# Kernel optimization log

Measured on AMD Instinct MI355X. Metric: run time of the kernel, lower is better.

The kernel has to match this reference:

```python
import jax, jax.numpy as jnp
import numpy as np

N, E, G, F_IN, H, C = 50000, 800000, 512, 128, 96, 10
BN_EPS = 1e-5


def _bn(x, w, b):
    # torch BatchNorm1d training-mode forward: batch stats, biased variance
    mu = jnp.mean(x, axis=0)
    var = jnp.var(x, axis=0)
    return (x - mu) * jax.lax.rsqrt(var + BN_EPS) * w + b


def setup_inputs() -> dict:
    key = jax.random.key(0)
    ks = iter(jax.random.split(key, 64))

    def rn(shape, s=0.05):
        return jax.random.normal(next(ks), shape, jnp.float32) * s

    inp = {
        "x": jax.random.normal(next(ks), (N, F_IN), jnp.float32),
        "edge_index": jax.random.randint(next(ks), (2, E), 0, N, dtype=jnp.int32),
        "batch": jnp.sort(jax.random.randint(next(ks), (N,), 0, G, dtype=jnp.int32)),
        "bn_feat_w": jnp.ones((F_IN,), jnp.float32),
        "bn_feat_b": jnp.full((F_IN,), 1e-4, jnp.float32),
        "Wf": rn((F_IN, H)), "bf": jnp.zeros((H,), jnp.float32),
        "bn_fc_w": jnp.ones((H,), jnp.float32),
        "bn_fc_b": jnp.full((H,), 1e-4, jnp.float32),
        "Wl": rn((H, H)), "bl": jnp.zeros((H,), jnp.float32),
        "bn_hid_w": jnp.ones((H,), jnp.float32),
        "bn_hid_b": jnp.full((H,), 1e-4, jnp.float32),
        "Wc": rn((H, C)), "bc": jnp.zeros((C,), jnp.float32),
    }
    for i in range(3):
        inp[f"W1_{i}"] = rn((H, H)); inp[f"b1_{i}"] = jnp.zeros((H,), jnp.float32)
        inp[f"bnw_{i}"] = jnp.ones((H,), jnp.float32)
        inp[f"bnb_{i}"] = jnp.full((H,), 1e-4, jnp.float32)
        inp[f"W2_{i}"] = rn((H, H)); inp[f"b2_{i}"] = jnp.zeros((H,), jnp.float32)
    return inp


def reference(x, edge_index, batch, bn_feat_w, bn_feat_b, Wf, bf,
              W1_0, b1_0, bnw_0, bnb_0, W2_0, b2_0,
              W1_1, b1_1, bnw_1, bnb_1, W2_1, b2_1,
              W1_2, b1_2, bnw_2, bnb_2, W2_2, b2_2,
              bn_fc_w, bn_fc_b, Wl, bl, bn_hid_w, bn_hid_b, Wc, bc):
    src, dst = edge_index[0], edge_index[1]
    h = _bn(x, bn_feat_w, bn_feat_b)
    # GCNConv(gfn=True): pure linear feature transform, no propagation
    h = jax.nn.relu(h @ Wf + bf)
    gin_params = [
        (W1_0, b1_0, bnw_0, bnb_0, W2_0, b2_0),
        (W1_1, b1_1, bnw_1, bnb_1, W2_1, b2_1),
        (W1_2, b1_2, bnw_2, bnb_2, W2_2, b2_2),
    ]
    for W1, b1, bw, bb, W2, b2 in gin_params:
        # GIN: (1+eps)*x + sum-aggregate of neighbor features (eps=0)
        agg = jax.ops.segment_sum(h[src], dst, num_segments=N)  # [N, H]
        m = h + agg
        m = jax.nn.relu(_bn(m @ W1 + b1, bw, bb))
        h = jax.nn.relu(m @ W2 + b2)
    # global_add_pool over graphs
    g = jax.ops.segment_sum(h, batch, num_segments=G)  # [G, H]
    g = jax.nn.relu(_bn(g, bn_fc_w, bn_fc_b) @ Wl + bl)
    g = _bn(g, bn_hid_w, bn_hid_b)
    logits = g @ Wc + bc
    return jax.nn.log_softmax(logits, axis=-1)
```

## Files before the change

### kernel.cpp

```cpp
#include <hip/hip_runtime.h>

#define N_NODES 50000
#define N_EDGES 800000
#define N_GRAPHS 512
#define F_IN 128
#define HDIM 96
#define NCLS 10
#define BN_EPS 1e-5f

#define NPB 128
#define NBUCK2 ((N_NODES + NPB - 1) / NPB)
#define NEB 128
#define EPB ((N_EDGES + NEB - 1) / NEB)

typedef unsigned int u32;
typedef unsigned short u16;
typedef __attribute__((ext_vector_type(8))) short bf16x8;
typedef __attribute__((ext_vector_type(4))) float f32x4;

__device__ __forceinline__ u16 f2bf(float f) {
    u32 u = __float_as_uint(f);
    u32 r = (u + 0x7fffu + ((u >> 16) & 1u)) >> 16;
    return (u16)r;
}
__device__ __forceinline__ float bflo(u32 w) { return __uint_as_float(w << 16); }
__device__ __forceinline__ float bfhi(u32 w) { return __uint_as_float(w & 0xffff0000u); }

template<int NC>
__global__ __launch_bounds__(256) void colstats4_kernel(const float* __restrict__ in,
                                                        float* __restrict__ stats,
                                                        int nrows) {
    constexpr int CG  = NC / 4;
    constexpr int RPB = 256 / CG;
    const int cg = threadIdx.x % CG;
    const int rg = threadIdx.x / CG;
    float4 s = make_float4(0.f, 0.f, 0.f, 0.f);
    float4 q = make_float4(0.f, 0.f, 0.f, 0.f);
    for (int r = blockIdx.x * RPB + rg; r < nrows; r += gridDim.x * RPB) {
        float4 v = *(const float4*)&in[(size_t)r * NC + cg * 4];
        s.x += v.x; s.y += v.y; s.z += v.z; s.w += v.w;
        q.x += v.x * v.x; q.y += v.y * v.y; q.z += v.z * v.z; q.w += v.w * v.w;
    }
    __shared__ float ss[RPB][NC], sq[RPB][NC];
    *(float4*)&ss[rg][cg * 4] = s;
    *(float4*)&sq[rg][cg * 4] = q;
    __syncthreads();
    if (threadIdx.x < NC) {
        float a = 0.f, b = 0.f;
        #pragma unroll
        for (int r = 0; r < RPB; r++) { a += ss[r][threadIdx.x]; b += sq[r][threadIdx.x]; }
        atomicAdd(&stats[threadIdx.x],      a);
        atomicAdd(&stats[NC + threadIdx.x], b);
    }
}

template<int NC>
__global__ __launch_bounds__(2*NC) void colstats_kernel(const float* __restrict__ in,
                                                        float* __restrict__ stats,
                                                        int nrows) {
    const int col  = threadIdx.x % NC;
    const int half = threadIdx.x / NC;
    float s = 0.f, ss = 0.f;
    for (int r = blockIdx.x * 2 + half; r < nrows; r += gridDim.x * 2) {
        float v = in[(size_t)r * NC + col];
        s += v; ss += v * v;
    }
    __shared__ float shs[2][NC], shq[2][NC];
    shs[half][col] = s; shq[half][col] = ss;
    __syncthreads();
    if (half == 0) {
        atomicAdd(&stats[col],      s  + shs[1][col]);
        atomicAdd(&stats[NC + col], ss + shq[1][col]);
    }
}

__global__ void finalize_bn_kernel(const float* __restrict__ stats,
                                   const float* __restrict__ w,
                                   const float* __restrict__ b,
                                   float* __restrict__ ac, int ncols, float inv_n) {
    int k = blockIdx.x * blockDim.x + threadIdx.x;
    if (k < ncols) {
        float mu  = stats[k] * inv_n;
        float var = stats[ncols + k] * inv_n - mu * mu;
        float a   = w[k] * rsqrtf(var + BN_EPS);
        ac[k]         = a;
        ac[ncols + k] = b[k] - mu * a;
    }
}

template<int KDIM, bool FOLD>
__global__ __launch_bounds__(256) void wprep_kernel(const float* __restrict__ W,
                                                    const float* __restrict__ bias,
                                                    const float* __restrict__ ac,
                                                    u16* __restrict__ wtb,
                                                    float* __restrict__ bmod) {
    int i = blockIdx.x * 256 + threadIdx.x;
    if (i < KDIM * 96) {
        int k = i / 96, n = i % 96;
        float v = W[i];
        if constexpr (FOLD) v *= ac[k];
        wtb[n * KDIM + k] = f2bf(v);
    }
    if (blockIdx.x == 0 && threadIdx.x < 96) {
        float b = bias[threadIdx.x];
        if constexpr (FOLD) {
            for (int k = 0; k < KDIM; k++) b += ac[KDIM + k] * W[k * 96 + threadIdx.x];
        }
        bmod[threadIdx.x] = b;
    }
}

__global__ __launch_bounds__(1024) void scan1_kernel(const int* __restrict__ in,
                                                     int* __restrict__ tmp,
                                                     int* __restrict__ partial, int n) {
    __shared__ int sh[1024];
    const int i = blockIdx.x * 1024 + threadIdx.x;
    const int d = (i < n) ? in[i] : 0;
    sh[threadIdx.x] = d;
    __syncthreads();
    for (int off = 1; off < 1024; off <<= 1) {
        int v = 0;
        if (threadIdx.x >= off) v = sh[threadIdx.x - off];
        __syncthreads();
        sh[threadIdx.x] += v;
        __syncthreads();
    }
    if (i < n) tmp[i] = sh[threadIdx.x] - d;
    if (threadIdx.x == 1023) partial[blockIdx.x] = sh[1023];
}

__global__ void scan2_kernel(int* __restrict__ partial, int nparts) {
    const int t = threadIdx.x;
    int d = (t < nparts) ? partial[t] : 0;
    int v = d;
    for (int off = 1; off < 64; off <<= 1) {
        int u = __shfl_up(v, off, 64);
        if (t >= off) v += u;
    }
    if (t < nparts) partial[t] = v - d;
}

__global__ __launch_bounds__(1024) void scan3_rowptr_kernel(const int* __restrict__ tmp,
                                                            const int* __restrict__ partial,
                                                            const int* __restrict__ deg,
                                                            int* __restrict__ row_ptr, int n) {
    const int i = blockIdx.x * 1024 + threadIdx.x;
    if (i < n) {
        int v = tmp[i] + partial[blockIdx.x];
        row_ptr[i] = v;
        if (i == n - 1) row_ptr[n] = v + deg[i];
    }
}

__global__ __launch_bounds__(1024) void scan3_kernel(const int* __restrict__ tmp,
                                                     const int* __restrict__ partial,
                                                     int* __restrict__ out, int n) {
    const int i = blockIdx.x * 1024 + threadIdx.x;
    if (i < n) out[i] = tmp[i] + partial[blockIdx.x];
}

__global__ __launch_bounds__(256) void count_kernel(const int* __restrict__ dst,
                                                    int* __restrict__ deg,
                                                    int* __restrict__ cnt ) {
    __shared__ int lc[NBUCK2];
    for (int i = threadIdx.x; i < NBUCK2; i += 256) lc[i] = 0;
    __syncthreads();
    const int lo = blockIdx.x * EPB;
    const int hi = min(lo + EPB, N_EDGES);
    for (int e = lo + threadIdx.x; e < hi; e += 256) {
        int d = dst[e];
        atomicAdd(&lc[d / NPB], 1);
        atomicAdd(&deg[d], 1);
    }
    __syncthreads();
    for (int i = threadIdx.x; i < NBUCK2; i += 256)
        cnt[i * NEB + blockIdx.x] = lc[i];
}

__global__ __launch_bounds__(256) void distribute_kernel(const int* __restrict__ src,
                                                         const int* __restrict__ dst,
                                                         const int* __restrict__ ofs,
                                                         u32* __restrict__ ebuf) {
    __shared__ int lofs[NBUCK2];
    for (int i = threadIdx.x; i < NBUCK2; i += 256) lofs[i] = ofs[i * NEB + blockIdx.x];
    __syncthreads();
    const int lo = blockIdx.x * EPB;
    const int hi = min(lo + EPB, N_EDGES);
    for (int e = lo + threadIdx.x; e < hi; e += 256) {
        int d = dst[e];
        int q = atomicAdd(&lofs[d / NPB], 1);
        ebuf[q] = ((u32)src[e] << 7) | (u32)(d & (NPB - 1));
    }
}

__global__ __launch_bounds__(256) void bucket_fill_kernel(const u32* __restrict__ ebuf,
                                                          const int* __restrict__ ofs,
                                                          const int* __restrict__ row_ptr,
                                                          int* __restrict__ csr) {
    __shared__ int cur[NPB];
    const int p    = blockIdx.x;
    const int base = p * NPB;
    const int nn   = min(NPB, N_NODES - base);
    for (int i = threadIdx.x; i < nn; i += 256) cur[i] = row_ptr[base + i];
    __syncthreads();
    const int e0 = ofs[p * NEB];
    const int e1 = (p + 1 < NBUCK2) ? ofs[(p + 1) * NEB] : N_EDGES;
    for (int e = e0 + threadIdx.x; e < e1; e += 256) {
        u32 v = ebuf[e];
        int pos = atomicAdd(&cur[v & (NPB - 1)], 1);
        csr[pos] = (int)(v >> 7);
    }
}

__global__ __launch_bounds__(192) void agg_kernel(const u16* __restrict__ hb,
                                                  const int* __restrict__ row_ptr,
                                                  const int* __restrict__ csr,
                                                  u16* __restrict__ mb, int n) {
    const int jj   = threadIdx.x % 12;
    const int node = blockIdx.x * 16 + threadIdx.x / 12;
    if (node >= n) return;
    const int p0 = row_ptr[node], p1 = row_ptr[node + 1];
    uint4 sv = *(const uint4*)&hb[(size_t)node * 96 + jj * 8];
    float a0 = bflo(sv.x), a1 = bfhi(sv.x), a2 = bflo(sv.y), a3 = bfhi(sv.y);
    float a4 = bflo(sv.z), a5 = bfhi(sv.z), a6 = bflo(sv.w), a7 = bfhi(sv.w);
    int p = p0;
    for (; p + 8 <= p1; p += 8) {
        int s0 = csr[p],     s1 = csr[p + 1], s2 = csr[p + 2], s3 = csr[p + 3];
        int s4 = csr[p + 4], s5 = csr[p + 5], s6 = csr[p + 6], s7 = csr[p + 7];
        uint4 v0 = *(const uint4*)&hb[(size_t)s0 * 96 + jj * 8];
        uint4 v1 = *(const uint4*)&hb[(size_t)s1 * 96 + jj * 8];
        uint4 v2 = *(const uint4*)&hb[(size_t)s2 * 96 + jj * 8];
        uint4 v3 = *(const uint4*)&hb[(size_t)s3 * 96 + jj * 8];
        uint4 v4 = *(const uint4*)&hb[(size_t)s4 * 96 + jj * 8];
        uint4 v5 = *(const uint4*)&hb[(size_t)s5 * 96 + jj * 8];
        uint4 v6 = *(const uint4*)&hb[(size_t)s6 * 96 + jj * 8];
        uint4 v7 = *(const uint4*)&hb[(size_t)s7 * 96 + jj * 8];
        a0 += ((bflo(v0.x) + bflo(v1.x)) + (bflo(v2.x) + bflo(v3.x)))
            + ((bflo(v4.x) + bflo(v5.x)) + (bflo(v6.x) + bflo(v7.x)));
        a1 += ((bfhi(v0.x) + bfhi(v1.x)) + (bfhi(v2.x) + bfhi(v3.x)))
            + ((bfhi(v4.x) + bfhi(v5.x)) + (bfhi(v6.x) + bfhi(v7.x)));
        a2 += ((bflo(v0.y) + bflo(v1.y)) + (bflo(v2.y) + bflo(v3.y)))
            + ((bflo(v4.y) + bflo(v5.y)) + (bflo(v6.y) + bflo(v7.y)));
        a3 += ((bfhi(v0.y) + bfhi(v1.y)) + (bfhi(v2.y) + bfhi(v3.y)))
            + ((bfhi(v4.y) + bfhi(v5.y)) + (bfhi(v6.y) + bfhi(v7.y)));
        a4 += ((bflo(v0.z) + bflo(v1.z)) + (bflo(v2.z) + bflo(v3.z)))
            + ((bflo(v4.z) + bflo(v5.z)) + (bflo(v6.z) + bflo(v7.z)));
        a5 += ((bfhi(v0.z) + bfhi(v1.z)) + (bfhi(v2.z) + bfhi(v3.z)))
            + ((bfhi(v4.z) + bfhi(v5.z)) + (bfhi(v6.z) + bfhi(v7.z)));
        a6 += ((bflo(v0.w) + bflo(v1.w)) + (bflo(v2.w) + bflo(v3.w)))
            + ((bflo(v4.w) + bflo(v5.w)) + (bflo(v6.w) + bflo(v7.w)));
        a7 += ((bfhi(v0.w) + bfhi(v1.w)) + (bfhi(v2.w) + bfhi(v3.w)))
            + ((bfhi(v4.w) + bfhi(v5.w)) + (bfhi(v6.w) + bfhi(v7.w)));
    }
    for (; p + 4 <= p1; p += 4) {
        int s0 = csr[p], s1 = csr[p + 1], s2 = csr[p + 2], s3 = csr[p + 3];
        uint4 v0 = *(const uint4*)&hb[(size_t)s0 * 96 + jj * 8];
        uint4 v1 = *(const uint4*)&hb[(size_t)s1 * 96 + jj * 8];
        uint4 v2 = *(const uint4*)&hb[(size_t)s2 * 96 + jj * 8];
        uint4 v3 = *(const uint4*)&hb[(size_t)s3 * 96 + jj * 8];
        a0 += (bflo(v0.x) + bflo(v1.x)) + (bflo(v2.x) + bflo(v3.x));
        a1 += (bfhi(v0.x) + bfhi(v1.x)) + (bfhi(v2.x) + bfhi(v3.x));
        a2 += (bflo(v0.y) + bflo(v1.y)) + (bflo(v2.y) + bflo(v3.y));
        a3 += (bfhi(v0.y) + bfhi(v1.y)) + (bfhi(v2.y) + bfhi(v3.y));
        a4 += (bflo(v0.z) + bflo(v1.z)) + (bflo(v2.z) + bflo(v3.z));
        a5 += (bfhi(v0.z) + bfhi(v1.z)) + (bfhi(v2.z) + bfhi(v3.z));
        a6 += (bflo(v0.w) + bflo(v1.w)) + (bflo(v2.w) + bflo(v3.w));
        a7 += (bfhi(v0.w) + bfhi(v1.w)) + (bfhi(v2.w) + bfhi(v3.w));
    }
    for (; p < p1; p++) {
        int s = csr[p];
        uint4 v = *(const uint4*)&hb[(size_t)s * 96 + jj * 8];
        a0 += bflo(v.x); a1 += bfhi(v.x); a2 += bflo(v.y); a3 += bfhi(v.y);
        a4 += bflo(v.z); a5 += bfhi(v.z); a6 += bflo(v.w); a7 += bfhi(v.w);
    }
    uint4 o;
    o.x = (u32)f2bf(a0) | ((u32)f2bf(a1) << 16);
    o.y = (u32)f2bf(a2) | ((u32)f2bf(a3) << 16);
    o.z = (u32)f2bf(a4) | ((u32)f2bf(a5) << 16);
    o.w = (u32)f2bf(a6) | ((u32)f2bf(a7) << 16);
    *(uint4*)&mb[(size_t)node * 96 + jj * 8] = o;
}

template<int KDIM, bool IN_F32, bool IN_AFF_RELU, bool OUT_RELU, bool STATS, bool OUT_BF16, bool POOL>
__global__ __launch_bounds__(256) void mmx_kernel(const void* __restrict__ in_,
                                                  const u16* __restrict__ wt,
                                                  const float* __restrict__ bias,
                                                  const float* __restrict__ ac,
                                                  void* __restrict__ out_,
                                                  float* __restrict__ stats,
                                                  const int* __restrict__ batch,
                                                  int nrows) {
    constexpr int KP = KDIM + 8;
    constexpr int KB = KDIM / 32;
    __shared__ u16 wlds[96 * KP];
    __shared__ u16 alds[64 * KP];
    __shared__ float sred[2][4][96];
    const int tid = threadIdx.x;

    for (int i = tid; i < 96 * (KDIM / 8); i += 256) {
        int nn = i / (KDIM / 8), c8 = i % (KDIM / 8);
        *(uint4*)&wlds[nn * KP + c8 * 8] = *(const uint4*)&wt[nn * KDIM + c8 * 8];
    }

    const int w    = tid >> 6;
    const int lane = tid & 63;
    const int r16  = lane & 15;
    const int kg   = lane >> 4;
    const int m0   = w * 16;
    float bn[6];
    #pragma unroll
    for (int nt = 0; nt < 6; nt++) bn[nt] = bias[nt * 16 + r16];
    float scol[6] = {0,0,0,0,0,0}, qcol[6] = {0,0,0,0,0,0};

    const int nchunks = (nrows + 63) / 64;
    for (int chunk = blockIdx.x; chunk < nchunks; chunk += gridDim.x) {
        const int row0 = chunk * 64;
        __syncthreads();
        if constexpr (IN_F32) {
            const float* inf = (const float*)in_;
            for (int i = tid; i < 64 * (KDIM / 4); i += 256) {
                int r = i / (KDIM / 4), c4 = i % (KDIM / 4);
                int gr = row0 + r;
                float4 v = (gr < nrows) ? *(const float4*)&inf[(size_t)gr * KDIM + c4 * 4]
                                        : make_float4(0.f, 0.f, 0.f, 0.f);
                ushort4 o; o.x = f2bf(v.x); o.y = f2bf(v.y); o.z = f2bf(v.z); o.w = f2bf(v.w);
                *(ushort4*)&alds[r * KP + c4 * 4] = o;
            }
        } else {
            const u16* inb = (const u16*)in_;
            for (int i = tid; i < 64 * (KDIM / 8); i += 256) {
                int r = i / (KDIM / 8), c8 = i % (KDIM / 8);
                int gr = row0 + r;
                uint4 v = (gr < nrows) ? *(const uint4*)&inb[(size_t)gr * KDIM + c8 * 8]
                                       : make_uint4(0u, 0u, 0u, 0u);
                if constexpr (IN_AFF_RELU) {
                    u32 words[4] = {v.x, v.y, v.z, v.w};
                    #pragma unroll
                    for (int t2 = 0; t2 < 4; t2++) {
                        int k0 = c8 * 8 + t2 * 2;
                        float lo = fmaxf(bflo(words[t2]) * ac[k0]     + ac[KDIM + k0],     0.f);
                        float hi = fmaxf(bfhi(words[t2]) * ac[k0 + 1] + ac[KDIM + k0 + 1], 0.f);
                        words[t2] = (u32)f2bf(lo) | ((u32)f2bf(hi) << 16);
                    }
                    v.x = words[0]; v.y = words[1]; v.z = words[2]; v.w = words[3];
                }
                *(uint4*)&alds[r * KP + c8 * 8] = v;
            }
        }
        __syncthreads();

        bf16x8 af[KB];
        #pragma unroll
        for (int kb = 0; kb < KB; kb++)
            af[kb] = *(const bf16x8*)&alds[(m0 + r16) * KP + kb * 32 + kg * 8];

        f32x4 acc[6];
        #pragma unroll
        for (int nt = 0; nt < 6; nt++) acc[nt] = (f32x4){bn[nt], bn[nt], bn[nt], bn[nt]};
        #pragma unroll
        for (int kb = 0; kb < KB; kb++) {
            #pragma unroll
            for (int nt = 0; nt < 6; nt++) {
                bf16x8 bfr = *(const bf16x8*)&wlds[(nt * 16 + r16) * KP + kb * 32 + kg * 8];
                acc[nt] = __builtin_amdgcn_mfma_f32_16x16x32_bf16(af[kb], bfr, acc[nt], 0, 0, 0);
            }
        }

        const int gr0  = row0 + m0 + kg * 4;
        const bool full = (gr0 + 3 < nrows);
        if constexpr (POOL) {
            float* gbuf = (float*)out_;
            int bl = -1, bh = -2;
            if (full) { bl = batch[gr0]; bh = batch[gr0 + 3]; }
            #pragma unroll
            for (int nt = 0; nt < 6; nt++) {
                float v0 = acc[nt][0], v1 = acc[nt][1], v2 = acc[nt][2], v3 = acc[nt][3];
                if constexpr (OUT_RELU) {
                    v0 = fmaxf(v0, 0.f); v1 = fmaxf(v1, 0.f);
                    v2 = fmaxf(v2, 0.f); v3 = fmaxf(v3, 0.f);
                }
                const int n = nt * 16 + r16;
                if (full) {
                    if (bl == bh) {
                        atomicAdd(&gbuf[(size_t)bl * 96 + n], (v0 + v1) + (v2 + v3));
                    } else {
                        atomicAdd(&gbuf[(size_t)batch[gr0]     * 96 + n], v0);
                        atomicAdd(&gbuf[(size_t)batch[gr0 + 1] * 96 + n], v1);
                        atomicAdd(&gbuf[(size_t)batch[gr0 + 2] * 96 + n], v2);
                        atomicAdd(&gbuf[(size_t)batch[gr0 + 3] * 96 + n], v3);
                    }
                } else {
                    if (gr0     < nrows) atomicAdd(&gbuf[(size_t)batch[gr0]     * 96 + n], v0);
                    if (gr0 + 1 < nrows) atomicAdd(&gbuf[(size_t)batch[gr0 + 1] * 96 + n], v1);
                    if (gr0 + 2 < nrows) atomicAdd(&gbuf[(size_t)batch[gr0 + 2] * 96 + n], v2);
                }
            }
        } else {
            #pragma unroll
            for (int nt = 0; nt < 6; nt++) {
                float v[4] = {acc[nt][0], acc[nt][1], acc[nt][2], acc[nt][3]};
                if constexpr (OUT_RELU) {
                    #pragma unroll
                    for (int rr = 0; rr < 4; rr++) v[rr] = fmaxf(v[rr], 0.f);
                }
                const int n = nt * 16 + r16;
                #pragma unroll
                for (int rr = 0; rr < 4; rr++) {
                    const int gr = gr0 + rr;
                    if (full || gr < nrows) {
                        if constexpr (OUT_BF16) ((u16*)out_)[(size_t)gr * 96 + n] = f2bf(v[rr]);
                        else                    ((float*)out_)[(size_t)gr * 96 + n] = v[rr];
                        if constexpr (STATS) { scol[nt] += v[rr]; qcol[nt] += v[rr] * v[rr]; }
                    }
                }
            }
        }
    }

    if constexpr (STATS) {
        #pragma unroll
        for (int nt = 0; nt < 6; nt++) {
            scol[nt] += __shfl_xor(scol[nt], 16);
            scol[nt] += __shfl_xor(scol[nt], 32);
            qcol[nt] += __shfl_xor(qcol[nt], 16);
            qcol[nt] += __shfl_xor(qcol[nt], 32);
        }
        __syncthreads();
        if (kg == 0) {
            #pragma unroll
            for (int nt = 0; nt < 6; nt++) {
                sred[0][w][nt * 16 + r16] = scol[nt];
                sred[1][w][nt * 16 + r16] = qcol[nt];
            }
        }
        __syncthreads();
        if (tid < 96) {
            float a = sred[0][0][tid] + sred[0][1][tid] + sred[0][2][tid] + sred[0][3][tid];
            float b = sred[1][0][tid] + sred[1][1][tid] + sred[1][2][tid] + sred[1][3][tid];
            atomicAdd(&stats[tid],      a);
            atomicAdd(&stats[96 + tid], b);
        }
    }
}

template<int KDIM, bool IN_AFF, bool IN_RELU, bool OUT_RELU, bool STATS>
__global__ __launch_bounds__(192) void mm_kernel(const float* __restrict__ in,
                                                 const float* __restrict__ W,
                                                 const float* __restrict__ bias,
                                                 const float* __restrict__ ac,
                                                 float* __restrict__ out,
                                                 float* __restrict__ stats, int nrows) {
    constexpr int KG = KDIM / 4;
    __shared__ float ws[KDIM][96];
    __shared__ float xs[32][KDIM];
    const int tid = threadIdx.x;
    const int cg  = tid % 24;
    const int rg  = tid / 24;
    for (int i = tid; i < KDIM * 24; i += 192) {
        int k = i / 24, c4 = i % 24;
        *(float4*)&ws[k][c4 * 4] = *(const float4*)&W[(size_t)k * 96 + c4 * 4];
    }
    const float4 bj = *(const float4*)&bias[cg * 4];
    float s0=0,s1=0,s2=0,s3=0, q0=0,q1=0,q2=0,q3=0;
    const int nchunks = (nrows + 31) / 32;
    for (int chunk = blockIdx.x; chunk < nchunks; chunk += gridDim.x) {
        const int row0 = chunk * 32;
        __syncthreads();
        for (int i = tid; i < 32 * KG; i += 192) {
            int r = i / KG, g = i % KG;
            int gr = row0 + r;
            float4 v = make_float4(0.f, 0.f, 0.f, 0.f);
            if (gr < nrows) v = *(const float4*)&in[(size_t)gr * KDIM + g * 4];
            if constexpr (IN_AFF) {
                float4 a = *(const float4*)&ac[g * 4];
                float4 c = *(const float4*)&ac[KDIM + g * 4];
                v.x = v.x * a.x + c.x; v.y = v.y * a.y + c.y;
                v.z = v.z * a.z + c.z; v.w = v.w * a.w + c.w;
            }
            if constexpr (IN_RELU) {
                v.x = fmaxf(v.x, 0.f); v.y = fmaxf(v.y, 0.f);
                v.z = fmaxf(v.z, 0.f); v.w = fmaxf(v.w, 0.f);
            }
            *(float4*)&xs[r][4 * (g ^ (r & 7))] = v;
        }
        __syncthreads();
        float acc[4][4];
        #pragma unroll
        for (int m = 0; m < 4; m++) {
            acc[m][0] = bj.x; acc[m][1] = bj.y; acc[m][2] = bj.z; acc[m][3] = bj.w;
        }
        #pragma unroll 4
        for (int g = 0; g < KG; g++) {
            const int xi = 4 * (g ^ rg);
            float4 xv0 = *(const float4*)&xs[rg     ][xi];
            float4 xv1 = *(const float4*)&xs[rg +  8][xi];
            float4 xv2 = *(const float4*)&xs[rg + 16][xi];
            float4 xv3 = *(const float4*)&xs[rg + 24][xi];
            #pragma unroll
            for (int i = 0; i < 4; i++) {
                float4 wv = *(const float4*)&ws[g * 4 + i][cg * 4];
                float x0 = (i==0)?xv0.x:(i==1)?xv0.y:(i==2)?xv0.z:xv0.w;
                float x1 = (i==0)?xv1.x:(i==1)?xv1.y:(i==2)?xv1.z:xv1.w;
                float x2 = (i==0)?xv2.x:(i==1)?xv2.y:(i==2)?xv2.z:xv2.w;
                float x3 = (i==0)?xv3.x:(i==1)?xv3.y:(i==2)?xv3.z:xv3.w;
                acc[0][0] = fmaf(x0, wv.x, acc[0][0]); acc[0][1] = fmaf(x0, wv.y, acc[0][1]);
                acc[0][2] = fmaf(x0, wv.z, acc[0][2]); acc[0][3] = fmaf(x0, wv.w, acc[0][3]);
                acc[1][0] = fmaf(x1, wv.x, acc[1][0]); acc[1][1] = fmaf(x1, wv.y, acc[1][1]);
                acc[1][2] = fmaf(x1, wv.z, acc[1][2]); acc[1][3] = fmaf(x1, wv.w, acc[1][3]);
                acc[2][0] = fmaf(x2, wv.x, acc[2][0]); acc[2][1] = fmaf(x2, wv.y, acc[2][1]);
                acc[2][2] = fmaf(x2, wv.z, acc[2][2]); acc[2][3] = fmaf(x2, wv.w, acc[2][3]);
                acc[3][0] = fmaf(x3, wv.x, acc[3][0]); acc[3][1] = fmaf(x3, wv.y, acc[3][1]);
                acc[3][2] = fmaf(x3, wv.z, acc[3][2]); acc[3][3] = fmaf(x3, wv.w, acc[3][3]);
            }
        }
        #pragma unroll
        for (int m = 0; m < 4; m++) {
            const int gr = row0 + rg + 8 * m;
            if (gr < nrows) {
                float4 o = make_float4(acc[m][0], acc[m][1], acc[m][2], acc[m][3]);
                if constexpr (OUT_RELU) {
                    o.x = fmaxf(o.x, 0.f); o.y = fmaxf(o.y, 0.f);
                    o.z = fmaxf(o.z, 0.f); o.w = fmaxf(o.w, 0.f);
                }
                *(float4*)&out[(size_t)gr * 96 + cg * 4] = o;
                if constexpr (STATS) {
                    s0 += o.x; q0 += o.x * o.x; s1 += o.y; q1 += o.y * o.y;
                    s2 += o.z; q2 += o.z * o.z; s3 += o.w; q3 += o.w * o.w;
                }
            }
        }
    }
    if constexpr (STATS) {
        __syncthreads();
        float* rs = &xs[0][0];
        float* rq = rs + 8 * 96;
        rs[rg * 96 + cg * 4 + 0] = s0; rs[rg * 96 + cg * 4 + 1] = s1;
        rs[rg * 96 + cg * 4 + 2] = s2; rs[rg * 96 + cg * 4 + 3] = s3;
        rq[rg * 96 + cg * 4 + 0] = q0; rq[rg * 96 + cg * 4 + 1] = q1;
        rq[rg * 96 + cg * 4 + 2] = q2; rq[rg * 96 + cg * 4 + 3] = q3;
        __syncthreads();
        if (tid < 96) {
            float a = 0.f, b = 0.f;
            #pragma unroll
            for (int r = 0; r < 8; r++) { a += rs[r * 96 + tid]; b += rq[r * 96 + tid]; }
            atomicAdd(&stats[tid],      a);
            atomicAdd(&stats[96 + tid], b);
        }
    }
}

__global__ void head_kernel(const float* __restrict__ g1, const float* __restrict__ ac,
                            const float* __restrict__ Wc, const float* __restrict__ bc,
                            float* __restrict__ out, int ngraphs) {
    int gi = blockIdx.x * blockDim.x + threadIdx.x;
    if (gi >= ngraphs) return;
    float v[NCLS];
    #pragma unroll
    for (int c = 0; c < NCLS; c++) v[c] = bc[c];
    for (int k = 0; k < HDIM; k++) {
        float x = g1[(size_t)gi * HDIM + k] * ac[k] + ac[HDIM + k];
        #pragma unroll
        for (int c = 0; c < NCLS; c++) v[c] = fmaf(x, Wc[k * NCLS + c], v[c]);
    }
    float mx = v[0];
    #pragma unroll
    for (int c = 1; c < NCLS; c++) mx = fmaxf(mx, v[c]);
    float sum = 0.f;
    #pragma unroll
    for (int c = 0; c < NCLS; c++) sum += expf(v[c] - mx);
    float lse = mx + logf(sum);
    #pragma unroll
    for (int c = 0; c < NCLS; c++) out[(size_t)gi * NCLS + c] = v[c] - lse;
}

extern "C" void kernel_launch(void* const* d_in, const int* in_sizes, int n_in,
                              void* d_out, int out_size, void* d_ws, size_t ws_size,
                              hipStream_t stream) {
    const float* x         = (const float*)d_in[0];
    const int*   ei        = (const int*)  d_in[1];
    const int*   batch     = (const int*)  d_in[2];
    const float* bn_feat_w = (const float*)d_in[3];
    const float* bn_feat_b = (const float*)d_in[4];
    const float* Wf        = (const float*)d_in[5];
    const float* bfv       = (const float*)d_in[6];
    const float* bn_fc_w   = (const float*)d_in[7];
    const float* bn_fc_b   = (const float*)d_in[8];
    const float* Wl        = (const float*)d_in[9];
    const float* bl        = (const float*)d_in[10];
    const float* bn_hid_w  = (const float*)d_in[11];
    const float* bn_hid_b  = (const float*)d_in[12];
    const float* Wc        = (const float*)d_in[13];
    const float* bc        = (const float*)d_in[14];
    float* out = (float*)d_out;

    char* p = (char*)d_ws;
    auto alloc = [&](size_t bytes) { char* q = p; p += (bytes + 255) & ~(size_t)255; return q; };
    u16*   hb     = (u16*)  alloc((size_t)N_NODES * HDIM * 2);
    u16*   mb     = (u16*)  alloc((size_t)N_NODES * HDIM * 2);
    float* g      = (float*)alloc((size_t)N_GRAPHS * HDIM * 4);
    float* g1     = (float*)alloc((size_t)N_GRAPHS * HDIM * 4);
    float* statsX = (float*)alloc(2 * F_IN * 4);
    float* acX    = (float*)alloc(2 * F_IN * 4);
    float* statsT = (float*)alloc(2 * HDIM * 4);
    float* acT    = (float*)alloc(2 * HDIM * 4);
    float* statsG = (float*)alloc(2 * HDIM * 4);
    float* acG    = (float*)alloc(2 * HDIM * 4);
    float* statsG1= (float*)alloc(2 * HDIM * 4);
    float* acHid  = (float*)alloc(2 * HDIM * 4);
    u16*   wtF    = (u16*)  alloc(96 * F_IN * 2);
    float* bFmod  = (float*)alloc(96 * 4);
    u16*   wt1[3]; u16* wt2[3]; float* b1mod[3]; float* b2mod[3];
    for (int l = 0; l < 3; l++) {
        wt1[l] = (u16*)alloc(96 * HDIM * 2); b1mod[l] = (float*)alloc(96 * 4);
        wt2[l] = (u16*)alloc(96 * HDIM * 2); b2mod[l] = (float*)alloc(96 * 4);
    }
    int* deg      = (int*)alloc((size_t)N_NODES * 4);
    int* row_ptr  = (int*)alloc((size_t)(N_NODES + 1) * 4);
    int* csr      = (int*)alloc((size_t)N_EDGES * 4);
    int* stmp     = (int*)alloc((size_t)N_NODES * 4);
    int* spart    = (int*)alloc(64 * 4);
    int* cnt      = (int*)alloc((size_t)NBUCK2 * NEB * 4);
    int* ofs      = (int*)alloc((size_t)NBUCK2 * NEB * 4);
    int* stmp2    = (int*)alloc((size_t)NBUCK2 * NEB * 4);
    int* spart2   = (int*)alloc(64 * 4);
    u32* ebuf     = (u32*)alloc((size_t)N_EDGES * 4);

    const int* srcp = ei;
    const int* dstp = ei + N_EDGES;

    const int nch64  = (N_NODES + 63) / 64;
    const int gridF  = (nch64 < 768) ? nch64 : 768;
    const int grid96 = (nch64 < 1024) ? nch64 : 1024;
    const int gridG  = (N_GRAPHS + 31) / 32;
    const int nscan  = (N_NODES + 1023) / 1024;
    const int ncb    = NBUCK2 * NEB;
    const int nscan2 = (ncb + 1023) / 1024;

    hipMemsetAsync(statsX, 0, 2 * F_IN * 4, stream);
    colstats4_kernel<F_IN><<<256, 256, 0, stream>>>(x, statsX, N_NODES);
    finalize_bn_kernel<<<1, F_IN, 0, stream>>>(statsX, bn_feat_w, bn_feat_b, acX, F_IN, 1.0f / N_NODES);
    wprep_kernel<F_IN, true><<<(F_IN * 96 + 255) / 256, 256, 0, stream>>>(Wf, bfv, acX, wtF, bFmod);
    mmx_kernel<F_IN, true, false, true, false, true, false><<<gridF, 256, 0, stream>>>(x, wtF, bFmod, nullptr, hb, nullptr, nullptr, N_NODES);

    for (int l = 0; l < 3; l++) {
        wprep_kernel<HDIM, false><<<(HDIM * 96 + 255) / 256, 256, 0, stream>>>((const float*)d_in[15 + 6 * l], (const float*)d_in[16 + 6 * l], nullptr, wt1[l], b1mod[l]);
        wprep_kernel<HDIM, false><<<(HDIM * 96 + 255) / 256, 256, 0, stream>>>((const float*)d_in[19 + 6 * l], (const float*)d_in[20 + 6 * l], nullptr, wt2[l], b2mod[l]);
    }

    hipMemsetAsync(deg, 0, (size_t)N_NODES * 4, stream);
    count_kernel<<<NEB, 256, 0, stream>>>(dstp, deg, cnt);
    scan1_kernel<<<nscan, 1024, 0, stream>>>(deg, stmp, spart, N_NODES);
    scan2_kernel<<<1, 64, 0, stream>>>(spart, nscan);
    scan3_rowptr_kernel<<<nscan, 1024, 0, stream>>>(stmp, spart, deg, row_ptr, N_NODES);
    scan1_kernel<<<nscan2, 1024, 0, stream>>>(cnt, stmp2, spart2, ncb);
    scan2_kernel<<<1, 64, 0, stream>>>(spart2, nscan2);
    scan3_kernel<<<nscan2, 1024, 0, stream>>>(stmp2, spart2, ofs, ncb);
    distribute_kernel<<<NEB, 256, 0, stream>>>(srcp, dstp, ofs, ebuf);
    bucket_fill_kernel<<<NBUCK2, 256, 0, stream>>>(ebuf, ofs, row_ptr, csr);

    hipMemsetAsync(g, 0, (size_t)N_GRAPHS * HDIM * 4, stream);

    for (int l = 0; l < 3; l++) {
        const float* bw = (const float*)d_in[17 + 6 * l];
        const float* bb = (const float*)d_in[18 + 6 * l];
        agg_kernel<<<(N_NODES + 15) / 16, 192, 0, stream>>>(hb, row_ptr, csr, mb, N_NODES);
        hipMemsetAsync(statsT, 0, 2 * HDIM * 4, stream);
        mmx_kernel<HDIM, false, false, false, true, true, false><<<grid96, 256, 0, stream>>>(mb, wt1[l], b1mod[l], nullptr, mb, statsT, nullptr, N_NODES);
        finalize_bn_kernel<<<1, HDIM, 0, stream>>>(statsT, bw, bb, acT, HDIM, 1.0f / N_NODES);
        if (l < 2) {
            mmx_kernel<HDIM, false, true, true, false, true, false><<<grid96, 256, 0, stream>>>(mb, wt2[l], b2mod[l], acT, hb, nullptr, nullptr, N_NODES);
        } else {
            mmx_kernel<HDIM, false, true, true, false, false, true><<<grid96, 256, 0, stream>>>(mb, wt2[l], b2mod[l], acT, g, nullptr, batch, N_NODES);
        }
    }

    hipMemsetAsync(statsG, 0, 2 * HDIM * 4, stream);
    colstats_kernel<HDIM><<<64, 2 * HDIM, 0, stream>>>(g, statsG, N_GRAPHS);
    finalize_bn_kernel<<<1, HDIM, 0, stream>>>(statsG, bn_fc_w, bn_fc_b, acG, HDIM, 1.0f / N_GRAPHS);
    hipMemsetAsync(statsG1, 0, 2 * HDIM * 4, stream);
    mm_kernel<HDIM, true, false, true, true><<<gridG, 192, 0, stream>>>(g, Wl, bl, acG, g1, statsG1, N_GRAPHS);
    finalize_bn_kernel<<<1, HDIM, 0, stream>>>(statsG1, bn_hid_w, bn_hid_b, acHid, HDIM, 1.0f / N_GRAPHS);

    head_kernel<<<2, 256, 0, stream>>>(g1, acHid, Wc, bc, out, N_GRAPHS);
}
```

Measured before the change: 371.5 us.

## Merge weight-prep launches, fold scan2 into scan3, coalesce memsets, fp32 intermediate

All seven weight-prep launches become one kernel. The separate scan2 kernels go away: each scan3 block sums the preceding partials with a wavefront reduction. All zeroing memsets are grouped into one contiguous region cleared once, with per-layer stats buffers. The first GIN matmul now writes fp32 into a new buffer instead of bf16 in place, and the second matmul reads fp32 and applies the BN affine plus ReLU during load. Fewer launches cut host overhead, but the intermediate activation traffic doubles from bf16 to fp32.

```diff
diff --git a/kernel.cpp b/kernel.cpp
--- a/kernel.cpp
+++ b/kernel.cpp
@@ -88,26 +88,53 @@
     }
 }
 
-template<int KDIM, bool FOLD>
-__global__ __launch_bounds__(256) void wprep_kernel(const float* __restrict__ W,
-                                                    const float* __restrict__ bias,
-                                                    const float* __restrict__ ac,
-                                                    u16* __restrict__ wtb,
-                                                    float* __restrict__ bmod) {
-    int i = blockIdx.x * 256 + threadIdx.x;
-    if (i < KDIM * 96) {
+#define WPF_BLOCKS 48
+#define WPH_BLOCKS 36
+__global__ __launch_bounds__(256) void wprep_all_kernel(
+        const float* __restrict__ Wf, const float* __restrict__ bf, const float* __restrict__ acX,
+        const float* __restrict__ W0a, const float* __restrict__ b0a,
+        const float* __restrict__ W0b, const float* __restrict__ b0b,
+        const float* __restrict__ W1a, const float* __restrict__ b1a,
+        const float* __restrict__ W1b, const float* __restrict__ b1b,
+        const float* __restrict__ W2a, const float* __restrict__ b2a,
+        const float* __restrict__ W2b, const float* __restrict__ b2b,
+        u16* __restrict__ wtF, float* __restrict__ bFm,
+        u16* __restrict__ wtbase, float* __restrict__ bmbase) {
+    const int tid = threadIdx.x;
+    int blk = blockIdx.x;
+    if (blk < WPF_BLOCKS) {
+        int i = blk * 256 + tid;
+        if (i < F_IN * 96) {
+            int k = i / 96, n = i % 96;
+            wtF[n * F_IN + k] = f2bf(Wf[i] * acX[k]);
+        }
+        if (blk == 0 && tid < 96) {
+            float b = bf[tid];
+            for (int k = 0; k < F_IN; k++) b += acX[F_IN + k] * Wf[k * 96 + tid];
+            bFm[tid] = b;
+        }
+        return;
+    }
+    blk -= WPF_BLOCKS;
+    const int s  = blk / WPH_BLOCKS;
+    const int b2 = blk % WPH_BLOCKS;
+    const float* W; const float* bias;
+    switch (s) {
+        case 0: W = W0a; bias = b0a; break;
+        case 1: W = W0b; bias = b0b; break;
+        case 2: W = W1a; bias = b1a; break;
+        case 3: W = W1b; bias = b1b; break;
+        case 4: W = W2a; bias = b2a; break;
+        default: W = W2b; bias = b2b; break;
+    }
+    u16*   wtb  = wtbase + (size_t)s * 96 * HDIM;
+    float* bmod = bmbase + (size_t)s * 96;
+    int i = b2 * 256 + tid;
+    if (i < HDIM * 96) {
         int k = i / 96, n = i % 96;
-        float v = W[i];
-        if constexpr (FOLD) v *= ac[k];
-        wtb[n * KDIM + k] = f2bf(v);
-    }
-    if (blockIdx.x == 0 && threadIdx.x < 96) {
-        float b = bias[threadIdx.x];
-        if constexpr (FOLD) {
-            for (int k = 0; k < KDIM; k++) b += ac[KDIM + k] * W[k * 96 + threadIdx.x];
-        }
-        bmod[threadIdx.x] = b;
-    }
+        wtb[n * HDIM + k] = f2bf(W[i]);
+    }
+    if (b2 == 0 && tid < 96) bmod[tid] = bias[tid];
 }
 
 __global__ __launch_bounds__(1024) void scan1_kernel(const int* __restrict__ in,
@@ -129,24 +156,21 @@
     if (threadIdx.x == 1023) partial[blockIdx.x] = sh[1023];
 }
 
-__global__ void scan2_kernel(int* __restrict__ partial, int nparts) {
-    const int t = threadIdx.x;
-    int d = (t < nparts) ? partial[t] : 0;
-    int v = d;
-    for (int off = 1; off < 64; off <<= 1) {
-        int u = __shfl_up(v, off, 64);
-        if (t >= off) v += u;
-    }
-    if (t < nparts) partial[t] = v - d;
-}
-
 __global__ __launch_bounds__(1024) void scan3_rowptr_kernel(const int* __restrict__ tmp,
                                                             const int* __restrict__ partial,
                                                             const int* __restrict__ deg,
-                                                            int* __restrict__ row_ptr, int n) {
+                                                            int* __restrict__ row_ptr,
+                                                            int n, int nparts) {
+    __shared__ int offs;
+    if (threadIdx.x < 64) {
+        int v = (threadIdx.x < blockIdx.x && threadIdx.x < nparts) ? partial[threadIdx.x] : 0;
+        for (int o = 32; o > 0; o >>= 1) v += __shfl_down(v, o, 64);
+        if (threadIdx.x == 0) offs = v;
+    }
+    __syncthreads();
     const int i = blockIdx.x * 1024 + threadIdx.x;
     if (i < n) {
-        int v = tmp[i] + partial[blockIdx.x];
+        int v = tmp[i] + offs;
         row_ptr[i] = v;
         if (i == n - 1) row_ptr[n] = v + deg[i];
     }
@@ -154,14 +178,22 @@
 
 __global__ __launch_bounds__(1024) void scan3_kernel(const int* __restrict__ tmp,
                                                      const int* __restrict__ partial,
-                                                     int* __restrict__ out, int n) {
+                                                     int* __restrict__ out,
+                                                     int n, int nparts) {
+    __shared__ int offs;
+    if (threadIdx.x < 64) {
+        int v = (threadIdx.x < blockIdx.x && threadIdx.x < nparts) ? partial[threadIdx.x] : 0;
+        for (int o = 32; o > 0; o >>= 1) v += __shfl_down(v, o, 64);
+        if (threadIdx.x == 0) offs = v;
+    }
+    __syncthreads();
     const int i = blockIdx.x * 1024 + threadIdx.x;
-    if (i < n) out[i] = tmp[i] + partial[blockIdx.x];
+    if (i < n) out[i] = tmp[i] + offs;
 }
 
 __global__ __launch_bounds__(256) void count_kernel(const int* __restrict__ dst,
                                                     int* __restrict__ deg,
-                                                    int* __restrict__ cnt ) {
+                                                    int* __restrict__ cnt) {
     __shared__ int lc[NBUCK2];
     for (int i = threadIdx.x; i < NBUCK2; i += 256) lc[i] = 0;
     __syncthreads();
@@ -323,6 +355,14 @@
                 int gr = row0 + r;
                 float4 v = (gr < nrows) ? *(const float4*)&inf[(size_t)gr * KDIM + c4 * 4]
                                         : make_float4(0.f, 0.f, 0.f, 0.f);
+                if constexpr (IN_AFF_RELU) {
+                    float4 a = *(const float4*)&ac[c4 * 4];
+                    float4 c = *(const float4*)&ac[KDIM + c4 * 4];
+                    v.x = fmaxf(v.x * a.x + c.x, 0.f);
+                    v.y = fmaxf(v.y * a.y + c.y, 0.f);
+                    v.z = fmaxf(v.z * a.z + c.z, 0.f);
+                    v.w = fmaxf(v.w * a.w + c.w, 0.f);
+                }
                 ushort4 o; o.x = f2bf(v.x); o.y = f2bf(v.y); o.z = f2bf(v.z); o.w = f2bf(v.w);
                 *(ushort4*)&alds[r * KP + c4 * 4] = o;
             }
@@ -595,26 +635,31 @@
 
     char* p = (char*)d_ws;
     auto alloc = [&](size_t bytes) { char* q = p; p += (bytes + 255) & ~(size_t)255; return q; };
+
+    char* zbase   = p;
+    float* statsX = (float*)alloc(2 * F_IN * 4);
+    float* statsT0= (float*)alloc(2 * HDIM * 4);
+    float* statsT1= (float*)alloc(2 * HDIM * 4);
+    float* statsT2= (float*)alloc(2 * HDIM * 4);
+    float* statsG = (float*)alloc(2 * HDIM * 4);
+    float* statsG1= (float*)alloc(2 * HDIM * 4);
+    int*   deg    = (int*)  alloc((size_t)N_NODES * 4);
+    float* g      = (float*)alloc((size_t)N_GRAPHS * HDIM * 4);
+    size_t zsize  = (size_t)(p - zbase);
+    float* statsT[3] = {statsT0, statsT1, statsT2};
+
     u16*   hb     = (u16*)  alloc((size_t)N_NODES * HDIM * 2);
     u16*   mb     = (u16*)  alloc((size_t)N_NODES * HDIM * 2);
-    float* g      = (float*)alloc((size_t)N_GRAPHS * HDIM * 4);
+    float* tf     = (float*)alloc((size_t)N_NODES * HDIM * 4);
     float* g1     = (float*)alloc((size_t)N_GRAPHS * HDIM * 4);
-    float* statsX = (float*)alloc(2 * F_IN * 4);
     float* acX    = (float*)alloc(2 * F_IN * 4);
-    float* statsT = (float*)alloc(2 * HDIM * 4);
     float* acT    = (float*)alloc(2 * HDIM * 4);
-    float* statsG = (float*)alloc(2 * HDIM * 4);
     float* acG    = (float*)alloc(2 * HDIM * 4);
-    float* statsG1= (float*)alloc(2 * HDIM * 4);
     float* acHid  = (float*)alloc(2 * HDIM * 4);
     u16*   wtF    = (u16*)  alloc(96 * F_IN * 2);
     float* bFmod  = (float*)alloc(96 * 4);
-    u16*   wt1[3]; u16* wt2[3]; float* b1mod[3]; float* b2mod[3];
-    for (int l = 0; l < 3; l++) {
-        wt1[l] = (u16*)alloc(96 * HDIM * 2); b1mod[l] = (float*)alloc(96 * 4);
-        wt2[l] = (u16*)alloc(96 * HDIM * 2); b2mod[l] = (float*)alloc(96 * 4);
-    }
-    int* deg      = (int*)alloc((size_t)N_NODES * 4);
+    u16*   wtH    = (u16*)  alloc((size_t)6 * 96 * HDIM * 2);
+    float* bmH    = (float*)alloc((size_t)6 * 96 * 4);
     int* row_ptr  = (int*)alloc((size_t)(N_NODES + 1) * 4);
     int* csr      = (int*)alloc((size_t)N_EDGES * 4);
     int* stmp     = (int*)alloc((size_t)N_NODES * 4);
@@ -636,48 +681,48 @@
     const int ncb    = NBUCK2 * NEB;
     const int nscan2 = (ncb + 1023) / 1024;
 
-    hipMemsetAsync(statsX, 0, 2 * F_IN * 4, stream);
+    hipMemsetAsync(zbase, 0, zsize, stream);
+
     colstats4_kernel<F_IN><<<256, 256, 0, stream>>>(x, statsX, N_NODES);
     finalize_bn_kernel<<<1, F_IN, 0, stream>>>(statsX, bn_feat_w, bn_feat_b, acX, F_IN, 1.0f / N_NODES);
-    wprep_kernel<F_IN, true><<<(F_IN * 96 + 255) / 256, 256, 0, stream>>>(Wf, bfv, acX, wtF, bFmod);
+    wprep_all_kernel<<<WPF_BLOCKS + 6 * WPH_BLOCKS, 256, 0, stream>>>(
+        Wf, bfv, acX,
+        (const float*)d_in[15], (const float*)d_in[16],
+        (const float*)d_in[19], (const float*)d_in[20],
+        (const float*)d_in[21], (const float*)d_in[22],
+        (const float*)d_in[25], (const float*)d_in[26],
+        (const float*)d_in[27], (const float*)d_in[28],
+        (const float*)d_in[31], (const float*)d_in[32],
+        wtF, bFmod, wtH, bmH);
     mmx_kernel<F_IN, true, false, true, false, true, false><<<gridF, 256, 0, stream>>>(x, wtF, bFmod, nullptr, hb, nullptr, nullptr, N_NODES);
 
-    for (int l = 0; l < 3; l++) {
-        wprep_kernel<HDIM, false><<<(HDIM * 96 + 255) / 256, 256, 0, stream>>>((const float*)d_in[15 + 6 * l], (const float*)d_in[16 + 6 * l], nullptr, wt1[l], b1mod[l]);
-        wprep_kernel<HDIM, false><<<(HDIM * 96 + 255) / 256, 256, 0, stream>>>((const float*)d_in[19 + 6 * l], (const float*)d_in[20 + 6 * l], nullptr, wt2[l], b2mod[l]);
-    }
-
-    hipMemsetAsync(deg, 0, (size_t)N_NODES * 4, stream);
     count_kernel<<<NEB, 256, 0, stream>>>(dstp, deg, cnt);
     scan1_kernel<<<nscan, 1024, 0, stream>>>(deg, stmp, spart, N_NODES);
-    scan2_kernel<<<1, 64, 0, stream>>>(spart, nscan);
-    scan3_rowptr_kernel<<<nscan, 1024, 0, stream>>>(stmp, spart, deg, row_ptr, N_NODES);
+    scan3_rowptr_kernel<<<nscan, 1024, 0, stream>>>(stmp, spart, deg, row_ptr, N_NODES, nscan);
     scan1_kernel<<<nscan2, 1024, 0, stream>>>(cnt, stmp2, spart2, ncb);
-    scan2_kernel<<<1, 64, 0, stream>>>(spart2, nscan2);
-    scan3_kernel<<<nscan2, 1024, 0, stream>>>(stmp2, spart2, ofs, ncb);
+    scan3_kernel<<<nscan2, 1024, 0, stream>>>(stmp2, spart2, ofs, ncb, nscan2);
     distribute_kernel<<<NEB, 256, 0, stream>>>(srcp, dstp, ofs, ebuf);
     bucket_fill_kernel<<<NBUCK2, 256, 0, stream>>>(ebuf, ofs, row_ptr, csr);
-
-    hipMemsetAsync(g, 0, (size_t)N_GRAPHS * HDIM * 4, stream);
 
     for (int l = 0; l < 3; l++) {
         const float* bw = (const float*)d_in[17 + 6 * l];
         const float* bb = (const float*)d_in[18 + 6 * l];
+        u16*   wt1 = wtH + (size_t)(2 * l)     * 96 * HDIM;
+        u16*   wt2 = wtH + (size_t)(2 * l + 1) * 96 * HDIM;
+        float* b1m = bmH + (size_t)(2 * l)     * 96;
+        float* b2m = bmH + (size_t)(2 * l + 1) * 96;
         agg_kernel<<<(N_NODES + 15) / 16, 192, 0, stream>>>(hb, row_ptr, csr, mb, N_NODES);
-        hipMemsetAsync(statsT, 0, 2 * HDIM * 4, stream);
-        mmx_kernel<HDIM, false, false, false, true, true, false><<<grid96, 256, 0, stream>>>(mb, wt1[l], b1mod[l], nullptr, mb, statsT, nullptr, N_NODES);
-        finalize_bn_kernel<<<1, HDIM, 0, stream>>>(statsT, bw, bb, acT, HDIM, 1.0f / N_NODES);
+        mmx_kernel<HDIM, false, false, false, true, false, false><<<grid96, 256, 0, stream>>>(mb, wt1, b1m, nullptr, tf, statsT[l], nullptr, N_NODES);
+        finalize_bn_kernel<<<1, HDIM, 0, stream>>>(statsT[l], bw, bb, acT, HDIM, 1.0f / N_NODES);
         if (l < 2) {
-            mmx_kernel<HDIM, false, true, true, false, true, false><<<grid96, 256, 0, stream>>>(mb, wt2[l], b2mod[l], acT, hb, nullptr, nullptr, N_NODES);
+            mmx_kernel<HDIM, true, true, true, false, true, false><<<grid96, 256, 0, stream>>>(tf, wt2, b2m, acT, hb, nullptr, nullptr, N_NODES);
         } else {
-            mmx_kernel<HDIM, false, true, true, false, false, true><<<grid96, 256, 0, stream>>>(mb, wt2[l], b2mod[l], acT, g, nullptr, batch, N_NODES);
-        }
-    }
-
-    hipMemsetAsync(statsG, 0, 2 * HDIM * 4, stream);
+            mmx_kernel<HDIM, true, true, true, false, false, true><<<grid96, 256, 0, stream>>>(tf, wt2, b2m, acT, g, nullptr, batch, N_NODES);
+        }
+    }
+
     colstats_kernel<HDIM><<<64, 2 * HDIM, 0, stream>>>(g, statsG, N_GRAPHS);
     finalize_bn_kernel<<<1, HDIM, 0, stream>>>(statsG, bn_fc_w, bn_fc_b, acG, HDIM, 1.0f / N_GRAPHS);
-    hipMemsetAsync(statsG1, 0, 2 * HDIM * 4, stream);
     mm_kernel<HDIM, true, false, true, true><<<gridG, 192, 0, stream>>>(g, Wl, bl, acG, g1, statsG1, N_GRAPHS);
     finalize_bn_kernel<<<1, HDIM, 0, stream>>>(statsG1, bn_hid_w, bn_hid_b, acHid, HDIM, 1.0f / N_GRAPHS);
 
```

After: 345.4 us. -7.0%, faster.
